# Performance work log

Measured on AMD Instinct MI355X. Metric: run time of the kernel, lower is better.

The kernel has to match this reference:

```python
import jax, jax.numpy as jnp
import numpy as np

# ---- hyperparameters (from pars / init_kwargs) ----
ALPHA = 0.9          # synaptic conductance decay (snn.Synaptic alpha)
BETA = 0.8           # membrane decay (snn.Synaptic beta)
BETA_PLUS = 0.9      # pre-synaptic trace decay
BETA_MINUS = 0.9     # post-synaptic trace decay
THRESHOLD = 1.0
W_MIN, W_MAX = 0.0, 1.0
A_PLUS, A_MINUS = 0.008, 0.0008
T, B, IN, N = 350, 128, 784, 400
SPIKE_P = 0.05       # Bernoulli firing probability of the rate-coded input


def setup_inputs() -> dict:
    key = jax.random.key(0)
    k_img, k_w = jax.random.split(key)
    # Poisson/Bernoulli rate-coded MNIST spike train [T, B, IN]
    image = (jax.random.uniform(k_img, (T, B, IN)) < SPIKE_P).astype(jnp.float32)
    # nn.Linear default init U(-1/sqrt(IN), 1/sqrt(IN)) then clamp to [w_min, w_max]
    s = 1.0 / np.sqrt(IN)
    W = jnp.clip(jax.random.uniform(k_w, (N, IN), minval=-s, maxval=s), W_MIN, W_MAX)
    return {"image": image, "W": W}


def reference(image, W):
    """Fused LIF (snntorch Synaptic, reset-by-subtraction) + STDP loop over T steps.

    Returns (W_final, mem_final, syn_final, total_spikes_per_neuron).
    """
    batch = image.shape[1]

    def step(carry, x_t):
        syn, mem, pre_tr, post_tr, W = carry
        # pre-synaptic trace: tr_t = beta_plus * tr_{t-1} + x_t
        pre_tr = BETA_PLUS * pre_tr + x_t                      # [B, IN]
        # linear projection (no bias)
        I_t = jnp.einsum('bi,ni->bn', x_t, W)                  # [B, N]
        # snntorch Synaptic: reset from pre-update mem, subtract mechanism
        reset = (mem > THRESHOLD).astype(mem.dtype)
        syn = ALPHA * syn + I_t
        mem = BETA * mem + syn - reset * THRESHOLD
        spk = (mem > THRESHOLD).astype(mem.dtype)              # [B, N]
        # post-synaptic trace
        post_tr = BETA_MINUS * post_tr + spk
        # STDP: potentiate on post spike x pre trace, depress on pre spike x post trace
        dW = (A_PLUS * jnp.einsum('bn,bi->ni', spk, pre_tr)
              - A_MINUS * jnp.einsum('bn,bi->ni', post_tr, x_t)) / batch
        W = jnp.clip(W + dW, W_MIN, W_MAX)
        return (syn, mem, pre_tr, post_tr, W), spk.sum(axis=0)

    syn0 = jnp.zeros((batch, N), image.dtype)
    mem0 = jnp.zeros((batch, N), image.dtype)
    pre0 = jnp.zeros((batch, IN), image.dtype)
    post0 = jnp.zeros((batch, N), image.dtype)

    (syn, mem, _, _, W_final), spk_counts = jax.lax.scan(
        step, (syn0, mem0, pre0, post0, W), image)
    return W_final, mem, syn, spk_counts.sum(axis=0)
```

## Files before the change

### kernel.cpp

```cpp
#include <hip/hip_runtime.h>
#include <hip/hip_bf16.h>


#define TT    350
#define BB    128
#define INF   784
#define NNEU  400
#define NS    2
#define NTHR  1024
#define LCAP  80

#define ALPHA 0.9f
#define BETA  0.8f
#define BPLUS 0.9f
#define BMIN  0.9f
#define CP    (0.008f/128.0f)
#define CM    (0.0008f/128.0f)

__device__ __forceinline__ float bf2f(__hip_bfloat16 v){ return __bfloat162float(v); }

__device__ __forceinline__ void barx(){
  asm volatile("s_waitcnt lgkmcnt(0)" ::: "memory");
  __builtin_amdgcn_s_barrier();
  __builtin_amdgcn_sched_barrier(0);
}

__global__ void k_pretr(const float* __restrict__ img, __hip_bfloat16* __restrict__ pre){
  int idx = blockIdx.x*blockDim.x + threadIdx.x;
  if (idx >= BB*INF) return;
  float v = 0.f;
  for (int t=0;t<TT;t++){
    v = BPLUS*v + img[(size_t)t*(BB*INF) + idx];
    pre[(size_t)t*(BB*INF) + idx] = __float2bfloat16(v);
  }
}

__global__ void k_S(const __hip_bfloat16* __restrict__ pre, float* __restrict__ S){
  int idx = blockIdx.x*blockDim.x + threadIdx.x;
  if (idx >= TT*INF) return;
  int t = idx / INF, i = idx - t*INF;
  const __hip_bfloat16* p = pre + (size_t)t*(BB*INF) + i;
  float s = 0.f;
  for (int b=0;b<BB;b++) s += bf2f(p[(size_t)b*INF]);
  S[idx] = s;
}

__global__ void k_masks(const float* __restrict__ img,
                        unsigned short* __restrict__ lists,
                        int* __restrict__ cnts,
                        unsigned int* __restrict__ collist){
  __shared__ unsigned long long rowbits[BB][13];
  __shared__ unsigned short buf[16][LCAP];
  const int t = blockIdx.x;
  const int tid = threadIdx.x, lane = tid & 63, w = tid >> 6;
  const float* base = img + (size_t)t*(BB*INF);

  for (int r8=0; r8<8; r8++){
    int r = w*8 + r8;
    const float* p = base + (size_t)r*INF;
    for (int c=0;c<13;c++){
      int i = c*64 + lane;
      bool a = (i < INF) && (p[i] > 0.f);
      unsigned long long bal = __ballot(a);
      if (lane == 0) rowbits[r][c] = bal;
    }
  }
  for (int r8=0; r8<8; r8++){
    int r = w*8 + r8;
    int cnt = 0;
    for (int c=0;c<13;c++){
      unsigned long long word = rowbits[r][c];
      int i = c*64 + lane;
      bool a = (word >> lane) & 1ull;
      int pos = cnt + __popcll(word & ((1ull<<lane)-1ull));
      if (a && pos < LCAP) buf[w][pos] = (unsigned short)(i<<3);
      cnt += __popcll(word);
    }
    for (int k = cnt + lane; k < LCAP; k += 64) buf[w][k] = (unsigned short)(INF<<3);
    if (lane == 0) cnts[t*BB + r] = (cnt < LCAP) ? cnt : LCAP;
    if (lane < LCAP/2)
      ((unsigned int*)(lists + (size_t)(t*BB + r)*LCAP))[lane] = ((unsigned int*)buf[w])[lane];
  }
  __syncthreads();
  if (tid < INF){
    int wsel = tid >> 6, bit = tid & 63;
    unsigned long long m0=0, m1=0;
    for (int b=0;b<64;b++) m0 |= ((rowbits[b][wsel]    >> bit) & 1ull) << b;
    for (int b=0;b<64;b++) m1 |= ((rowbits[64+b][wsel] >> bit) & 1ull) << b;
    int cnt = __popcll(m0) + __popcll(m1);
    unsigned int wd[8];
    wd[0] = (unsigned int)cnt; wd[1]=0;wd[2]=0;wd[3]=0;wd[4]=0;wd[5]=0;wd[6]=0;wd[7]=0;
    #pragma unroll
    for (int k=1;k<32;k++){
      int bb;
      if (m0){ bb = __builtin_ctzll(m0); m0 &= m0-1; }
      else if (m1){ bb = 64 + __builtin_ctzll(m1); m1 &= m1-1; }
      else bb = 128;
      wd[k>>2] |= ((unsigned int)bb) << ((k&3)*8);
    }
    uint4* dst = (uint4*)(collist + ((size_t)t*INF + tid)*8);
    uint4 lo; lo.x=wd[0]; lo.y=wd[1]; lo.z=wd[2]; lo.w=wd[3];
    uint4 hi; hi.x=wd[4]; hi.y=wd[5]; hi.z=wd[6]; hi.w=wd[7];
    dst[0]=lo; dst[1]=hi;
  }
}

__device__ __forceinline__ float potf(unsigned long long ma, unsigned long long mb,
                                      int pc, float Sv,
                                      const __hip_bfloat16* __restrict__ prt, int c){
  bool direct = (pc <= 64);
  unsigned long long m = direct ? ma : ~ma;
  unsigned long long n = direct ? mb : ~mb;
  float acc = 0.f;
  while (m){ int bb = __builtin_ctzll(m); m &= m-1; acc += bf2f(prt[(size_t)bb*INF + c]); }
  while (n){ int bb = __builtin_ctzll(n); n &= n-1; acc += bf2f(prt[(size_t)(64+bb)*INF + c]); }
  return direct ? acc : (Sv - acc);
}

#define G2(W) { float2 a_ = *(const float2*)((const char*)&Wp2[0] + ((W) & 0xffffu)); I0 += a_.x; I1 += a_.y; \
                float2 b_ = *(const float2*)((const char*)&Wp2[0] + ((W) >> 16));     I0 += b_.x; I1 += b_.y; }
#define GATHER8(V) { G2((V).x); G2((V).y); G2((V).z); G2((V).w); }

#define DEP4(W) { float2 p_; \
  p_ = postl[(W) & 0xffu];        d0 += p_.x; d1 += p_.y; \
  p_ = postl[((W)>>8) & 0xffu];   d0 += p_.x; d1 += p_.y; \
  p_ = postl[((W)>>16) & 0xffu];  d0 += p_.x; d1 += p_.y; \
  p_ = postl[(W)>>24];            d0 += p_.x; d1 += p_.y; }

__launch_bounds__(NTHR, 1)
__global__ void k_main(const float* __restrict__ Win,
                       const __hip_bfloat16* __restrict__ pre,
                       const float* __restrict__ S,
                       const unsigned short* __restrict__ lists,
                       const int* __restrict__ cnts,
                       const unsigned int* __restrict__ collist,
                       float* __restrict__ out){
  __shared__ float2 Wp2[800];
  __shared__ float2 postl[132];
  __shared__ unsigned long long smQ[2][2];
  __shared__ ulonglong2 mdiffL[2];
  __shared__ float cntS[2];

  const int tid  = threadIdx.x;
  const int lane = tid & 63;
  const int wv   = tid >> 6;
  const int q    = lane >> 3;
  const int b    = (wv << 3) | (lane & 7);
  const int n0   = blockIdx.x * NS;

  if (tid < 800){
    float2 w;
    w.x = (tid < INF) ? Win[(size_t)n0*INF + tid] : 0.f;
    w.y = (tid < INF) ? Win[(size_t)(n0+1)*INF + tid] : 0.f;
    Wp2[tid] = w;
  }
  if (tid < 132){ postl[tid].x = 0.f; postl[tid].y = 0.f; }
  if (tid < 2) cntS[tid] = 0.f;
  if (tid == 0){
    mdiffL[0].x = 0ull; mdiffL[0].y = 0ull;
    mdiffL[1].x = 0ull; mdiffL[1].y = 0ull;
  }

  const int  c0   = tid;
  const bool hasc = (c0 < INF);

  float syn0=0.f, mem0=0.f, syn1=0.f, mem1=0.f, sc0=0.f, sc1=0.f;
  float C0=0.f, C1=0.f;
  bool anyEver = false;

  uint4 lA = *(const uint4*)(lists + ((size_t)b)*LCAP + (size_t)q*8);
  int cn = cnts[b];
  uint4 cl0; cl0.x=0;cl0.y=0;cl0.z=0;cl0.w=0;
  float sv0 = 0.f;
  if (hasc){ cl0 = *(const uint4*)(collist + (size_t)c0*8); sv0 = S[c0]; }

  __syncthreads();

  for (int t=0; t<TT; t++){
    float I0 = 0.f, I1 = 0.f;
    GATHER8(lA);
    if (cn > 64 + q*8){
      uint4 lC = *(const uint4*)(lists + ((size_t)t*BB + b)*LCAP + 64 + (size_t)q*8);
      GATHER8(lC);
    }
    int tn = (t+1 < TT) ? t+1 : TT-1;
    uint4 lAn = *(const uint4*)(lists + ((size_t)tn*BB + b)*LCAP + (size_t)q*8);
    int cnn = cnts[tn*BB + b];
    uint4 cl0n = cl0; float sv0n = sv0;
    if (hasc){
      cl0n = *(const uint4*)(collist + ((size_t)tn*INF + c0)*8);
      sv0n = S[tn*INF + c0];
    }

    I0 += __shfl_xor(I0, 8); I0 += __shfl_xor(I0, 16); I0 += __shfl_xor(I0, 32);
    I1 += __shfl_xor(I1, 8); I1 += __shfl_xor(I1, 16); I1 += __shfl_xor(I1, 32);

    float r0 = (mem0 > 1.f) ? 1.f : 0.f;
    syn0 = ALPHA*syn0 + I0;
    mem0 = BETA*mem0 + syn0 - r0;
    float s0 = (mem0 > 1.f) ? 1.f : 0.f;
    float r1 = (mem1 > 1.f) ? 1.f : 0.f;
    syn1 = ALPHA*syn1 + I1;
    mem1 = BETA*mem1 + syn1 - r1;
    float s1 = (mem1 > 1.f) ? 1.f : 0.f;
    unsigned long long bal0 = __ballot(s0 > 0.5f);
    unsigned long long bal1 = __ballot(s1 > 0.5f);
    if (q == 0){
      sc0 += s0; sc1 += s1;
      float2 pv = postl[b];
      pv.x = fmaf(BMIN, pv.x, s0);
      pv.y = fmaf(BMIN, pv.y, s1);
      postl[b] = pv;
    }
    if (lane == 0){
      ((unsigned char*)smQ)[wv]      = (unsigned char)(bal0 & 0xffu);
      ((unsigned char*)smQ)[16 + wv] = (unsigned char)(bal1 & 0xffu);
    }
    barx();

    unsigned long long s00 = smQ[0][0], s01 = smQ[0][1];
    unsigned long long s10 = smQ[1][0], s11 = smQ[1][1];
    float sb0 = (float)(int)(s00 & 1ull);
    float sb1 = (float)(int)(s10 & 1ull);
    C0 = fmaf(BMIN, C0, sb0);
    C1 = fmaf(BMIN, C1, sb1);
    ulonglong2 mdv = mdiffL[t & 1];
    unsigned long long sf0 = (s00 & 1ull) ? ~s00 : s00;
    unsigned long long sf1 = (s00 & 1ull) ? ~s01 : s01;
    unsigned long long sg0 = (s10 & 1ull) ? ~s10 : s10;
    unsigned long long sg1 = (s10 & 1ull) ? ~s11 : s11;
    unsigned long long md0 = mdv.x | sf0 | sg0;
    unsigned long long md1 = mdv.y | sf1 | sg1;

    bool anyNow = ((s00|s01|s10|s11) != 0ull);
    bool runD = anyEver || anyNow;
    anyEver = runD;

    if (wv == 13){
      float2 a0 = postl[lane], a1 = postl[64 + lane];
      bool eq0 = (a0.x == C0) && (a0.y == C1);
      bool eq1 = (a1.x == C0) && (a1.y == C1);
      unsigned long long d0 = ~__ballot(eq0);
      unsigned long long d1 = ~__ballot(eq1);
      if (lane == 0){ mdiffL[(t+1)&1].x = d0; mdiffL[(t+1)&1].y = d1; }
    }

    if (runD && hasc){
      float d0, d1;
      float cntf = (float)(int)(cl0.x & 0xffu);
      if ((md0 | md1) == 0ull){
        d0 = C0 * cntf; d1 = C1 * cntf;
      } else {
        d0 = 0.f; d1 = 0.f;
        unsigned int w0_ = cl0.x;
        { float2 p_;
          p_ = postl[(w0_>>8) & 0xffu];  d0 += p_.x; d1 += p_.y;
          p_ = postl[(w0_>>16) & 0xffu]; d0 += p_.x; d1 += p_.y;
          p_ = postl[w0_>>24];           d0 += p_.x; d1 += p_.y; }
        DEP4(cl0.y); DEP4(cl0.z); DEP4(cl0.w);
        int cc_ = (int)(w0_ & 0xffu);
        if (cc_ > 15){
          uint4 e2_ = *(const uint4*)(collist + ((size_t)t*INF + c0)*8 + 4);
          DEP4(e2_.x); DEP4(e2_.y); DEP4(e2_.z); DEP4(e2_.w);
        }
      }
      int pc0 = __popcll(s00) + __popcll(s01);
      int pc1 = __popcll(s10) + __popcll(s11);
      const __hip_bfloat16* prt = pre + (size_t)t*(BB*INF);
      float pot0 = potf(s00, s01, pc0, sv0, prt, c0);
      float pot1 = potf(s10, s11, pc1, sv0, prt, c0);
      float2 wv_ = Wp2[c0];
      wv_.x = fminf(fmaxf(wv_.x + CP*pot0 - CM*d0, 0.f), 1.f);
      wv_.y = fminf(fmaxf(wv_.y + CP*pot1 - CM*d1, 0.f), 1.f);
      Wp2[c0] = wv_;
    }

    lA=lAn; cn=cnn; cl0=cl0n; sv0=sv0n;
    barx();
  }

  __syncthreads();
  if (tid < INF){
    float2 wvv = Wp2[tid];
    out[(size_t)n0*INF + tid]       = wvv.x;
    out[(size_t)(n0+1)*INF + tid]   = wvv.y;
  }
  if (q == 0){
    out[(size_t)NNEU*INF + (size_t)b*NNEU + n0]                        = mem0;
    out[(size_t)NNEU*INF + (size_t)b*NNEU + n0 + 1]                    = mem1;
    out[(size_t)NNEU*INF + (size_t)BB*NNEU + (size_t)b*NNEU + n0]      = syn0;
    out[(size_t)NNEU*INF + (size_t)BB*NNEU + (size_t)b*NNEU + n0 + 1]  = syn1;
    atomicAdd(&cntS[0], sc0);
    atomicAdd(&cntS[1], sc1);
  }
  __syncthreads();
  if (tid < 2) out[(size_t)NNEU*INF + 2*(size_t)BB*NNEU + n0 + tid] = cntS[tid];
}

extern "C" void kernel_launch(void* const* d_in, const int* in_sizes, int n_in,
                              void* d_out, int out_size, void* d_ws, size_t ws_size,
                              hipStream_t stream) {
  const float* img = (const float*)d_in[0];
  const float* W   = (const float*)d_in[1];
  float* out = (float*)d_out;

  char* ws = (char*)d_ws;
  __hip_bfloat16* pre  = (__hip_bfloat16*)ws;
  float*          S    = (float*)(ws + 70246400);
  unsigned short* lst  = (unsigned short*)(ws + 71344000);
  int*            cnts = (int*)(ws + 78512000);
  unsigned int*   coll = (unsigned int*)(ws + 78691200);

  k_pretr<<<(BB*INF + 255)/256, 256, 0, stream>>>(img, pre);
  k_masks<<<TT, NTHR, 0, stream>>>(img, lst, cnts, coll);
  k_S    <<<(TT*INF + 255)/256, 256, 0, stream>>>(pre, S);
  k_main <<<NNEU/NS, NTHR, 0, stream>>>(W, pre, S, lst, cnts, coll, out);
}
```

Baseline: 749.1 us.

## Use DPP row reduction for input current and drop uniform-trace depression shortcut

Remaps lanes so the 8 partial sums per batch row sit within DPP-reachable rows and reduces them with update_dpp instead of cross-lane shuffles, repacking the ballot bits to match the new layout. It also removes the shortcut that detected when all post traces were equal and replaced the depression gather with a multiply, along with the anyEver skip and the wave-13 comparison pass. Depression is now always computed through the full LDS gather. This trims per-step overhead and one wave's extra work, but every step now pays the gather cost even when the shortcut would have applied.

```diff
diff --git a/kernel.cpp b/kernel.cpp
--- a/kernel.cpp
+++ b/kernel.cpp
@@ -23,6 +23,13 @@
   asm volatile("s_waitcnt lgkmcnt(0)" ::: "memory");
   __builtin_amdgcn_s_barrier();
   __builtin_amdgcn_sched_barrier(0);
+}
+
+__device__ __forceinline__ float dppred(float x){
+  x += __int_as_float(__builtin_amdgcn_update_dpp(0, __float_as_int(x), 0x4E,  0xF, 0xF, true));
+  x += __int_as_float(__builtin_amdgcn_update_dpp(0, __float_as_int(x), 0x124, 0xF, 0xF, true));
+  x += __int_as_float(__builtin_amdgcn_update_dpp(0, __float_as_int(x), 0x128, 0xF, 0xF, true));
+  return x;
 }
 
 __global__ void k_pretr(const float* __restrict__ img, __hip_bfloat16* __restrict__ pre){
@@ -138,14 +145,13 @@
   __shared__ float2 Wp2[800];
   __shared__ float2 postl[132];
   __shared__ unsigned long long smQ[2][2];
-  __shared__ ulonglong2 mdiffL[2];
   __shared__ float cntS[2];
 
   const int tid  = threadIdx.x;
   const int lane = tid & 63;
   const int wv   = tid >> 6;
-  const int q    = lane >> 3;
-  const int b    = (wv << 3) | (lane & 7);
+  const int q    = (lane >> 1) & 7;
+  const int b    = (lane & 1) | (((lane >> 4) & 3) << 1) | (wv << 3);
   const int n0   = blockIdx.x * NS;
 
   if (tid < 800){
@@ -156,17 +162,11 @@
   }
   if (tid < 132){ postl[tid].x = 0.f; postl[tid].y = 0.f; }
   if (tid < 2) cntS[tid] = 0.f;
-  if (tid == 0){
-    mdiffL[0].x = 0ull; mdiffL[0].y = 0ull;
-    mdiffL[1].x = 0ull; mdiffL[1].y = 0ull;
-  }
 
   const int  c0   = tid;
   const bool hasc = (c0 < INF);
 
   float syn0=0.f, mem0=0.f, syn1=0.f, mem1=0.f, sc0=0.f, sc1=0.f;
-  float C0=0.f, C1=0.f;
-  bool anyEver = false;
 
   uint4 lA = *(const uint4*)(lists + ((size_t)b)*LCAP + (size_t)q*8);
   int cn = cnts[b];
@@ -192,8 +192,8 @@
       sv0n = S[tn*INF + c0];
     }
 
-    I0 += __shfl_xor(I0, 8); I0 += __shfl_xor(I0, 16); I0 += __shfl_xor(I0, 32);
-    I1 += __shfl_xor(I1, 8); I1 += __shfl_xor(I1, 16); I1 += __shfl_xor(I1, 32);
+    I0 = dppred(I0);
+    I1 = dppred(I1);
 
     float r0 = (mem0 > 1.f) ? 1.f : 0.f;
     syn0 = ALPHA*syn0 + I0;
@@ -208,61 +208,34 @@
     if (q == 0){
       sc0 += s0; sc1 += s1;
       float2 pv = postl[b];
-      pv.x = fmaf(BMIN, pv.x, s0);
-      pv.y = fmaf(BMIN, pv.y, s1);
+      pv.x = BMIN*pv.x + s0;
+      pv.y = BMIN*pv.y + s1;
       postl[b] = pv;
     }
     if (lane == 0){
-      ((unsigned char*)smQ)[wv]      = (unsigned char)(bal0 & 0xffu);
-      ((unsigned char*)smQ)[16 + wv] = (unsigned char)(bal1 & 0xffu);
+      unsigned int by0 = (unsigned int)((bal0 & 3ull) | ((bal0>>16)&3ull)<<2 |
+                                        ((bal0>>32)&3ull)<<4 | ((bal0>>48)&3ull)<<6);
+      unsigned int by1 = (unsigned int)((bal1 & 3ull) | ((bal1>>16)&3ull)<<2 |
+                                        ((bal1>>32)&3ull)<<4 | ((bal1>>48)&3ull)<<6);
+      ((unsigned char*)smQ)[wv]      = (unsigned char)by0;
+      ((unsigned char*)smQ)[16 + wv] = (unsigned char)by1;
     }
     barx();
 
     unsigned long long s00 = smQ[0][0], s01 = smQ[0][1];
     unsigned long long s10 = smQ[1][0], s11 = smQ[1][1];
-    float sb0 = (float)(int)(s00 & 1ull);
-    float sb1 = (float)(int)(s10 & 1ull);
-    C0 = fmaf(BMIN, C0, sb0);
-    C1 = fmaf(BMIN, C1, sb1);
-    ulonglong2 mdv = mdiffL[t & 1];
-    unsigned long long sf0 = (s00 & 1ull) ? ~s00 : s00;
-    unsigned long long sf1 = (s00 & 1ull) ? ~s01 : s01;
-    unsigned long long sg0 = (s10 & 1ull) ? ~s10 : s10;
-    unsigned long long sg1 = (s10 & 1ull) ? ~s11 : s11;
-    unsigned long long md0 = mdv.x | sf0 | sg0;
-    unsigned long long md1 = mdv.y | sf1 | sg1;
-
-    bool anyNow = ((s00|s01|s10|s11) != 0ull);
-    bool runD = anyEver || anyNow;
-    anyEver = runD;
-
-    if (wv == 13){
-      float2 a0 = postl[lane], a1 = postl[64 + lane];
-      bool eq0 = (a0.x == C0) && (a0.y == C1);
-      bool eq1 = (a1.x == C0) && (a1.y == C1);
-      unsigned long long d0 = ~__ballot(eq0);
-      unsigned long long d1 = ~__ballot(eq1);
-      if (lane == 0){ mdiffL[(t+1)&1].x = d0; mdiffL[(t+1)&1].y = d1; }
-    }
-
-    if (runD && hasc){
-      float d0, d1;
-      float cntf = (float)(int)(cl0.x & 0xffu);
-      if ((md0 | md1) == 0ull){
-        d0 = C0 * cntf; d1 = C1 * cntf;
-      } else {
-        d0 = 0.f; d1 = 0.f;
-        unsigned int w0_ = cl0.x;
-        { float2 p_;
-          p_ = postl[(w0_>>8) & 0xffu];  d0 += p_.x; d1 += p_.y;
-          p_ = postl[(w0_>>16) & 0xffu]; d0 += p_.x; d1 += p_.y;
-          p_ = postl[w0_>>24];           d0 += p_.x; d1 += p_.y; }
-        DEP4(cl0.y); DEP4(cl0.z); DEP4(cl0.w);
-        int cc_ = (int)(w0_ & 0xffu);
-        if (cc_ > 15){
-          uint4 e2_ = *(const uint4*)(collist + ((size_t)t*INF + c0)*8 + 4);
-          DEP4(e2_.x); DEP4(e2_.y); DEP4(e2_.z); DEP4(e2_.w);
-        }
+    if (hasc){
+      float d0=0.f, d1=0.f;
+      unsigned int w0_ = cl0.x;
+      { float2 p_;
+        p_ = postl[(w0_>>8) & 0xffu];  d0 += p_.x; d1 += p_.y;
+        p_ = postl[(w0_>>16) & 0xffu]; d0 += p_.x; d1 += p_.y;
+        p_ = postl[w0_>>24];           d0 += p_.x; d1 += p_.y; }
+      DEP4(cl0.y); DEP4(cl0.z); DEP4(cl0.w);
+      int cc_ = (int)(w0_ & 0xffu);
+      if (cc_ > 15){
+        uint4 e2_ = *(const uint4*)(collist + ((size_t)t*INF + c0)*8 + 4);
+        DEP4(e2_.x); DEP4(e2_.y); DEP4(e2_.z); DEP4(e2_.w);
       }
       int pc0 = __popcll(s00) + __popcll(s01);
       int pc1 = __popcll(s10) + __popcll(s11);
```

Result: faster. 711.6 us, median of 2 (-5.0%).
